# Kernel tuning notes

Measured on AMD Instinct MI355X. Metric: run time of the kernel, lower is better.

Reference implementation:

```python
import jax, jax.numpy as jnp
import numpy as np

E4M3_MAX = 448.0
M, K, N = 131072, 512, 512


def _round_to_fp8_e4m3(x):
    # Emulated round-to-nearest E4M3: 3 mantissa bits, exponent in [-7, 8]
    abs_x = jnp.abs(x)
    sign = jnp.sign(x)
    exponent = jnp.clip(jnp.floor(jnp.log2(jnp.maximum(abs_x, 2.0 ** -9))), -7.0, 8.0)
    pow2e = jnp.exp2(exponent)
    mantissa = jnp.round(abs_x / pow2e * 8.0) / 8.0  # jnp.round is half-to-even, matching torch.round
    return sign * mantissa * pow2e


def _quantize_e4m3(x, scale):
    scaled = jnp.clip(x * scale, -E4M3_MAX, E4M3_MAX)
    return _round_to_fp8_e4m3(scaled)


def _dynamic_scale(x):
    # FP8TensorMeta.compute_scale with a single amax in history: max_value / amax * 0.9
    amax = jnp.max(jnp.abs(x))
    return jnp.where(amax > 0, E4M3_MAX / amax * 0.9, 1.0)


def setup_inputs() -> dict:
    key = jax.random.key(0)
    k1, k2, k3 = jax.random.split(key, 3)
    bound = 1.0 / np.sqrt(K)  # kaiming_uniform(a=sqrt(5)) on [N,K] -> U(-1/sqrt(K), 1/sqrt(K))
    x = jax.random.normal(k1, (M, K), dtype=jnp.float32)
    weight = jax.random.uniform(k2, (N, K), dtype=jnp.float32, minval=-bound, maxval=bound)
    bias = jax.random.uniform(k3, (N,), dtype=jnp.float32, minval=-bound, maxval=bound)
    return {"x": x, "weight": weight, "bias": bias}


def reference(x, weight, bias):
    input_scale = _dynamic_scale(x)
    weight_scale = _dynamic_scale(weight)
    x_fp8 = _quantize_e4m3(x, input_scale)          # [M, K]
    w_fp8 = _quantize_e4m3(weight, weight_scale)    # [N, K]
    out = jnp.einsum("mk,nk->mn", x_fp8, w_fp8) + bias  # F.linear
    return out / (input_scale * weight_scale)
```

## Files before the change

kernel.cpp:

```cpp
#include <hip/hip_runtime.h>

typedef unsigned short u16;
typedef unsigned int u32;
typedef __attribute__((ext_vector_type(8))) short short8;
typedef __attribute__((ext_vector_type(4))) float f32x4;

__device__ __forceinline__ u16 quant_bf16(float v, float scale) {
  float sc = v * scale;
  sc = fminf(448.0f, fmaxf(-448.0f, sc));
  u32 b = __float_as_uint(sc);
  u32 sb = (b & 0x7f800000u) + 0x0A000000u;
  sb = sb < 0x46000000u ? 0x46000000u : sb;
  float mg = __uint_as_float(sb);
  float q = (fabsf(sc) + mg) - mg;
  u32 qb = __float_as_uint(q) | (b & 0x80000000u);
  return (u16)(qb >> 16);
}

__device__ __forceinline__ float block_max(float m) {
#pragma unroll
  for (int off = 32; off > 0; off >>= 1)
    m = fmaxf(m, __shfl_down(m, off, 64));
  __shared__ float sm[4];
  int wv = threadIdx.x >> 6;
  if ((threadIdx.x & 63) == 0) sm[wv] = m;
  __syncthreads();
  float r = fmaxf(fmaxf(sm[0], sm[1]), fmaxf(sm[2], sm[3]));
  __syncthreads();
  return r;
}

#define XBLOCKS 2048
#define WBLOCKS 64

__global__ void amax2_kernel(const float4* __restrict__ x, int nx4,
                             const float4* __restrict__ w, int nw4,
                             float* __restrict__ px, float* __restrict__ pw) {
  int bid = blockIdx.x;
  const float4* p;
  int n4, b, nb;
  float* dst;
  if (bid < XBLOCKS) { p = x; n4 = nx4; dst = px; b = bid; nb = XBLOCKS; }
  else { p = w; n4 = nw4; dst = pw; b = bid - XBLOCKS; nb = WBLOCKS; }
  float m = 0.0f;
  int stride = nb * 256;
  for (int i = b * 256 + threadIdx.x; i < n4; i += stride) {
    float4 v = p[i];
    m = fmaxf(m, fmaxf(fmaxf(fabsf(v.x), fabsf(v.y)), fmaxf(fabsf(v.z), fabsf(v.w))));
  }
  m = block_max(m);
  if (threadIdx.x == 0) dst[b] = m;
}

__global__ void scales_kernel(const float* __restrict__ px, const float* __restrict__ pw,
                              float* __restrict__ wsf) {
  int tid = threadIdx.x;
  float mx = 0.0f;
  for (int i = tid; i < XBLOCKS; i += 256) mx = fmaxf(mx, px[i]);
  mx = block_max(mx);
  float mw = tid < WBLOCKS ? pw[tid] : 0.0f;
  mw = block_max(mw);
  if (tid == 0) {
    float sx = mx > 0.0f ? 448.0f / mx * 0.9f : 1.0f;
    float sw = mw > 0.0f ? 448.0f / mw * 0.9f : 1.0f;
    wsf[2] = sx;
    wsf[3] = sw;
    wsf[4] = 1.0f / (sx * sw);
  }
}

__global__ void quant_w_kernel(const float* __restrict__ w, u16* __restrict__ wq,
                               const float* __restrict__ wsf) {
  const float sw = wsf[3];
  const int id = blockIdx.x * blockDim.x + threadIdx.x;
  const int kc = id >> 9;
  const int n = id & 511;
  const float4* src = (const float4*)(w + (size_t)n * 512 + kc * 8);
  const float4 a = src[0];
  const float4 b = src[1];
  uint4 r;
  r.x = (u32)quant_bf16(a.x, sw) | ((u32)quant_bf16(a.y, sw) << 16);
  r.y = (u32)quant_bf16(a.z, sw) | ((u32)quant_bf16(a.w, sw) << 16);
  r.z = (u32)quant_bf16(b.x, sw) | ((u32)quant_bf16(b.y, sw) << 16);
  r.w = (u32)quant_bf16(b.z, sw) | ((u32)quant_bf16(b.w, sw) << 16);
  *(uint4*)&wq[(size_t)kc * 4096 + n * 8] = r;
}

__global__ void __launch_bounds__(256, 2) gemm_kernel(const float* __restrict__ x,
                                                      const u16* __restrict__ wq,
                                                      const float* __restrict__ bias,
                                                      float* __restrict__ out,
                                                      const float* __restrict__ wsf) {
  __shared__ u16 As[2 * 4096];
  __shared__ u16 Bs[2 * 8192];
  const int tid = threadIdx.x;
  const int lane = tid & 63;
  const int wv = tid >> 6;
  const int quad = lane >> 4;
  const int lr = lane & 15;

  const int lin = blockIdx.x;
  const int xcd = lin & 7;
  const int jn = (lin >> 3) & 1;
  const int grp = lin >> 4;
  const int m0 = (grp * 8 + xcd) * 128;
  const int n0 = jn * 256;

  const float sx = wsf[2];
  const float inv = wsf[4];
  const int wm = (wv >> 1) * 64;
  const int wn = (wv & 1) * 128;
  const int xrow = tid >> 3;
  const int xcol = (tid & 7) * 4;
  const int aq = xcol >> 3;
  const int aoff = xcol & 7;

  f32x4 acc[4][8] = {};
  float4 xr[4];

  auto stageB = [&](int bu, int kt) {
#pragma unroll
    for (int i = 0; i < 4; ++i) {
      const u16* gp = wq + (size_t)(kt * 4 + wv) * 4096 + (size_t)n0 * 8 + (i * 64 + lane) * 8;
      u16* lp = &Bs[bu * 8192 + wv * 2048 + (i * 64 + lane) * 8];
      __builtin_amdgcn_global_load_lds((const __attribute__((address_space(1))) u32*)gp,
                                       (__attribute__((address_space(3))) u32*)lp, 16, 0, 0);
    }
  };
  auto loadX = [&](int kt) {
#pragma unroll
    for (int s = 0; s < 4; ++s) {
      const int r = s * 32 + xrow;
      xr[s] = *(const float4*)(x + (size_t)(m0 + r) * 512 + kt * 32 + xcol);
    }
  };
  auto writeA = [&](int bu) {
#pragma unroll
    for (int s = 0; s < 4; ++s) {
      const int r = s * 32 + xrow;
      uint2 pk;
      pk.x = (u32)quant_bf16(xr[s].x, sx) | ((u32)quant_bf16(xr[s].y, sx) << 16);
      pk.y = (u32)quant_bf16(xr[s].z, sx) | ((u32)quant_bf16(xr[s].w, sx) << 16);
      *(uint2*)&As[bu * 4096 + aq * 1024 + r * 8 + aoff] = pk;
    }
  };

  stageB(0, 0);
  loadX(0);
  writeA(0);
  __syncthreads();

  for (int kt = 0; kt < 16; ++kt) {
    const int cur = kt & 1;
    if (kt < 15) {
      loadX(kt + 1);
      stageB(cur ^ 1, kt + 1);
    }
    short8 af[4], bf[8];
#pragma unroll
    for (int mi = 0; mi < 4; ++mi)
      af[mi] = *(const short8*)&As[cur * 4096 + quad * 1024 + (wm + mi * 16 + lr) * 8];
#pragma unroll
    for (int ni = 0; ni < 8; ++ni)
      bf[ni] = *(const short8*)&Bs[cur * 8192 + quad * 2048 + (wn + ni * 16 + lr) * 8];
#pragma unroll
    for (int mi = 0; mi < 4; ++mi)
#pragma unroll
      for (int ni = 0; ni < 8; ++ni)
        acc[mi][ni] = __builtin_amdgcn_mfma_f32_16x16x32_bf16(af[mi], bf[ni], acc[mi][ni], 0, 0, 0);
    if (kt < 15) writeA(cur ^ 1);
    __syncthreads();
  }

  float bn[8];
#pragma unroll
  for (int ni = 0; ni < 8; ++ni) bn[ni] = bias[n0 + wn + ni * 16 + lr];
#pragma unroll
  for (int mi = 0; mi < 4; ++mi) {
    const int gr = m0 + wm + mi * 16 + quad * 4;
#pragma unroll
    for (int ni = 0; ni < 8; ++ni) {
      const int gc = n0 + wn + ni * 16 + lr;
#pragma unroll
      for (int j = 0; j < 4; ++j)
        out[(size_t)(gr + j) * 512 + gc] = (acc[mi][ni][j] + bn[ni]) * inv;
    }
  }
}

extern "C" void kernel_launch(void* const* d_in, const int* in_sizes, int n_in,
                              void* d_out, int out_size, void* d_ws, size_t ws_size,
                              hipStream_t stream) {
  const float* x = (const float*)d_in[0];
  const float* w = (const float*)d_in[1];
  const float* bias = (const float*)d_in[2];
  float* out = (float*)d_out;

  const int K = 512, N = 512;
  const int M = in_sizes[0] / K;

  float* ws_f = (float*)d_ws;
  float* px = ws_f + 16;
  float* pw = ws_f + 16 + XBLOCKS;
  u16* wq = (u16*)((char*)d_ws + 16384);

  hipLaunchKernelGGL(amax2_kernel, dim3(XBLOCKS + WBLOCKS), dim3(256), 0, stream,
                     (const float4*)x, (M * K) / 4, (const float4*)w, (N * K) / 4, px, pw);
  hipLaunchKernelGGL(scales_kernel, dim3(1), dim3(256), 0, stream, px, pw, ws_f);
  hipLaunchKernelGGL(quant_w_kernel, dim3((N * K / 8) / 256), dim3(256), 0, stream,
                     w, wq, ws_f);
  hipLaunchKernelGGL(gemm_kernel, dim3((M / 128) * 2), dim3(256), 0, stream,
                     x, wq, bias, out, ws_f);
}
```

Baseline: 571.7 us.

## Switch GEMM to native FP8 MFMA with hardware E4M3 conversion and 512-thread blocks

Activations and weights are now quantized with the hardware packed FP8 conversion builtin and stored as 8-bit values in shared memory. The GEMM uses fp8×fp8 MFMA instead of bf16 MFMA on emulated-FP8 values. Blocks grow to 512 threads, each wave computes a 64×64 tile, and per-thread staging work shrinks. This halves operand bytes in LDS and global weight traffic and uses the higher-rate FP8 matrix path. The cost is that the hardware E4M3 format may round tiny subnormal values slightly differently from the reference emulation.

```diff
diff --git a/kernel.cpp b/kernel.cpp
--- a/kernel.cpp
+++ b/kernel.cpp
@@ -2,19 +2,14 @@
 
 typedef unsigned short u16;
 typedef unsigned int u32;
-typedef __attribute__((ext_vector_type(8))) short short8;
+typedef unsigned char u8;
 typedef __attribute__((ext_vector_type(4))) float f32x4;
 
-__device__ __forceinline__ u16 quant_bf16(float v, float scale) {
-  float sc = v * scale;
-  sc = fminf(448.0f, fmaxf(-448.0f, sc));
-  u32 b = __float_as_uint(sc);
-  u32 sb = (b & 0x7f800000u) + 0x0A000000u;
-  sb = sb < 0x46000000u ? 0x46000000u : sb;
-  float mg = __uint_as_float(sb);
-  float q = (fabsf(sc) + mg) - mg;
-  u32 qb = __float_as_uint(q) | (b & 0x80000000u);
-  return (u16)(qb >> 16);
+template <bool HI>
+__device__ __forceinline__ u32 q2fp8(float a, float b, u32 old, float s) {
+  a = fminf(448.0f, fmaxf(-448.0f, a * s));
+  b = fminf(448.0f, fmaxf(-448.0f, b * s));
+  return (u32)__builtin_amdgcn_cvt_pk_fp8_f32(a, b, (int)old, HI);
 }
 
 __device__ __forceinline__ float block_max(float m) {
@@ -69,7 +64,7 @@
   }
 }
 
-__global__ void quant_w_kernel(const float* __restrict__ w, u16* __restrict__ wq,
+__global__ void quant_w_kernel(const float* __restrict__ w, u8* __restrict__ wq,
                                const float* __restrict__ wsf) {
   const float sw = wsf[3];
   const int id = blockIdx.x * blockDim.x + threadIdx.x;
@@ -78,21 +73,21 @@
   const float4* src = (const float4*)(w + (size_t)n * 512 + kc * 8);
   const float4 a = src[0];
   const float4 b = src[1];
-  uint4 r;
-  r.x = (u32)quant_bf16(a.x, sw) | ((u32)quant_bf16(a.y, sw) << 16);
-  r.y = (u32)quant_bf16(a.z, sw) | ((u32)quant_bf16(a.w, sw) << 16);
-  r.z = (u32)quant_bf16(b.x, sw) | ((u32)quant_bf16(b.y, sw) << 16);
-  r.w = (u32)quant_bf16(b.z, sw) | ((u32)quant_bf16(b.w, sw) << 16);
-  *(uint4*)&wq[(size_t)kc * 4096 + n * 8] = r;
-}
-
-__global__ void __launch_bounds__(256, 2) gemm_kernel(const float* __restrict__ x,
-                                                      const u16* __restrict__ wq,
+  uint2 r;
+  r.x = q2fp8<false>(a.x, a.y, 0u, sw);
+  r.x = q2fp8<true>(a.z, a.w, r.x, sw);
+  r.y = q2fp8<false>(b.x, b.y, 0u, sw);
+  r.y = q2fp8<true>(b.z, b.w, r.y, sw);
+  *(uint2*)&wq[(size_t)kc * 4096 + n * 8] = r;
+}
+
+__global__ void __launch_bounds__(512, 4) gemm_kernel(const float* __restrict__ x,
+                                                      const u8* __restrict__ wq,
                                                       const float* __restrict__ bias,
                                                       float* __restrict__ out,
                                                       const float* __restrict__ wsf) {
-  __shared__ u16 As[2 * 4096];
-  __shared__ u16 Bs[2 * 8192];
+  __shared__ __align__(16) u8 As[2 * 4096];
+  __shared__ __align__(16) u8 Bs[2 * 8192];
   const int tid = threadIdx.x;
   const int lane = tid & 63;
   const int wv = tid >> 6;
@@ -108,41 +103,35 @@
 
   const float sx = wsf[2];
   const float inv = wsf[4];
-  const int wm = (wv >> 1) * 64;
-  const int wn = (wv & 1) * 128;
-  const int xrow = tid >> 3;
-  const int xcol = (tid & 7) * 4;
-  const int aq = xcol >> 3;
-  const int aoff = xcol & 7;
-
-  f32x4 acc[4][8] = {};
-  float4 xr[4];
+  const int wm = (wv >> 2) * 64;
+  const int wn = (wv & 3) * 64;
+  const int xrow = tid >> 2;
+  const int xcol = (tid & 3) * 8;
+  const int aq = tid & 3;
+
+  f32x4 acc[4][4] = {};
+  float4 xr0, xr1;
 
   auto stageB = [&](int bu, int kt) {
-#pragma unroll
-    for (int i = 0; i < 4; ++i) {
-      const u16* gp = wq + (size_t)(kt * 4 + wv) * 4096 + (size_t)n0 * 8 + (i * 64 + lane) * 8;
-      u16* lp = &Bs[bu * 8192 + wv * 2048 + (i * 64 + lane) * 8];
-      __builtin_amdgcn_global_load_lds((const __attribute__((address_space(1))) u32*)gp,
-                                       (__attribute__((address_space(3))) u32*)lp, 16, 0, 0);
-    }
+    const int c = wv >> 1;
+    const int h = wv & 1;
+    const u8* gp = wq + (size_t)(kt * 4 + c) * 4096 + (size_t)n0 * 8 + h * 1024 + lane * 16;
+    u8* lp = &Bs[bu * 8192 + c * 2048 + h * 1024 + lane * 16];
+    __builtin_amdgcn_global_load_lds((const __attribute__((address_space(1))) u32*)gp,
+                                     (__attribute__((address_space(3))) u32*)lp, 16, 0, 0);
   };
   auto loadX = [&](int kt) {
-#pragma unroll
-    for (int s = 0; s < 4; ++s) {
-      const int r = s * 32 + xrow;
-      xr[s] = *(const float4*)(x + (size_t)(m0 + r) * 512 + kt * 32 + xcol);
-    }
+    const float* p = x + (size_t)(m0 + xrow) * 512 + kt * 32 + xcol;
+    xr0 = *(const float4*)p;
+    xr1 = *(const float4*)(p + 4);
   };
   auto writeA = [&](int bu) {
-#pragma unroll
-    for (int s = 0; s < 4; ++s) {
-      const int r = s * 32 + xrow;
-      uint2 pk;
-      pk.x = (u32)quant_bf16(xr[s].x, sx) | ((u32)quant_bf16(xr[s].y, sx) << 16);
-      pk.y = (u32)quant_bf16(xr[s].z, sx) | ((u32)quant_bf16(xr[s].w, sx) << 16);
-      *(uint2*)&As[bu * 4096 + aq * 1024 + r * 8 + aoff] = pk;
-    }
+    uint2 pk;
+    pk.x = q2fp8<false>(xr0.x, xr0.y, 0u, sx);
+    pk.x = q2fp8<true>(xr0.z, xr0.w, pk.x, sx);
+    pk.y = q2fp8<false>(xr1.x, xr1.y, 0u, sx);
+    pk.y = q2fp8<true>(xr1.z, xr1.w, pk.y, sx);
+    *(uint2*)&As[bu * 4096 + aq * 1024 + xrow * 8] = pk;
   };
 
   stageB(0, 0);
@@ -156,30 +145,30 @@
       loadX(kt + 1);
       stageB(cur ^ 1, kt + 1);
     }
-    short8 af[4], bf[8];
+    long af[4], bf[4];
 #pragma unroll
     for (int mi = 0; mi < 4; ++mi)
-      af[mi] = *(const short8*)&As[cur * 4096 + quad * 1024 + (wm + mi * 16 + lr) * 8];
-#pragma unroll
-    for (int ni = 0; ni < 8; ++ni)
-      bf[ni] = *(const short8*)&Bs[cur * 8192 + quad * 2048 + (wn + ni * 16 + lr) * 8];
+      af[mi] = *(const long*)&As[cur * 4096 + quad * 1024 + (wm + mi * 16 + lr) * 8];
+#pragma unroll
+    for (int ni = 0; ni < 4; ++ni)
+      bf[ni] = *(const long*)&Bs[cur * 8192 + quad * 2048 + (wn + ni * 16 + lr) * 8];
 #pragma unroll
     for (int mi = 0; mi < 4; ++mi)
 #pragma unroll
-      for (int ni = 0; ni < 8; ++ni)
-        acc[mi][ni] = __builtin_amdgcn_mfma_f32_16x16x32_bf16(af[mi], bf[ni], acc[mi][ni], 0, 0, 0);
+      for (int ni = 0; ni < 4; ++ni)
+        acc[mi][ni] = __builtin_amdgcn_mfma_f32_16x16x32_fp8_fp8(af[mi], bf[ni], acc[mi][ni], 0, 0, 0);
     if (kt < 15) writeA(cur ^ 1);
     __syncthreads();
   }
 
-  float bn[8];
-#pragma unroll
-  for (int ni = 0; ni < 8; ++ni) bn[ni] = bias[n0 + wn + ni * 16 + lr];
+  float bn[4];
+#pragma unroll
+  for (int ni = 0; ni < 4; ++ni) bn[ni] = bias[n0 + wn + ni * 16 + lr];
 #pragma unroll
   for (int mi = 0; mi < 4; ++mi) {
     const int gr = m0 + wm + mi * 16 + quad * 4;
 #pragma unroll
-    for (int ni = 0; ni < 8; ++ni) {
+    for (int ni = 0; ni < 4; ++ni) {
       const int gc = n0 + wn + ni * 16 + lr;
 #pragma unroll
       for (int j = 0; j < 4; ++j)
@@ -202,13 +191,13 @@
   float* ws_f = (float*)d_ws;
   float* px = ws_f + 16;
   float* pw = ws_f + 16 + XBLOCKS;
-  u16* wq = (u16*)((char*)d_ws + 16384);
+  u8* wq = (u8*)((char*)d_ws + 16384);
 
   hipLaunchKernelGGL(amax2_kernel, dim3(XBLOCKS + WBLOCKS), dim3(256), 0, stream,
                      (const float4*)x, (M * K) / 4, (const float4*)w, (N * K) / 4, px, pw);
   hipLaunchKernelGGL(scales_kernel, dim3(1), dim3(256), 0, stream, px, pw, ws_f);
   hipLaunchKernelGGL(quant_w_kernel, dim3((N * K / 8) / 256), dim3(256), 0, stream,
                      w, wq, ws_f);
-  hipLaunchKernelGGL(gemm_kernel, dim3((M / 128) * 2), dim3(256), 0, stream,
+  hipLaunchKernelGGL(gemm_kernel, dim3((M / 128) * 2), dim3(512), 0, stream,
                      x, wq, bias, out, ws_f);
 }
```

Result: faster. 542.5 us (-5.1%).
